# Optimization experiments

Hardware: AMD Instinct MI355X
Metric: run time of the kernel (lower is better)

Reference implementation:

```python
import jax, jax.numpy as jnp
import numpy as np

L, B, E, H, HID = 2048, 4, 512, 8, 2048
HD = E // H


def setup_inputs() -> dict:
    key = jax.random.key(0)
    ks = jax.random.split(key, 6)
    s = 0.02
    x = jax.random.normal(ks[0], (L, B, E), jnp.float32)
    in_proj_w = jax.random.normal(ks[1], (3 * E, E), jnp.float32) * s
    in_proj_b = jnp.zeros((3 * E,), jnp.float32)
    out_w = jax.random.normal(ks[2], (E, E), jnp.float32) * s
    out_b = jnp.zeros((E,), jnp.float32)
    w1 = jax.random.normal(ks[3], (HID, E), jnp.float32) * s  # torch Linear: (out, in)
    b1 = jnp.zeros((HID,), jnp.float32)
    w2 = jax.random.normal(ks[4], (E, HID), jnp.float32) * s
    b2 = jnp.zeros((E,), jnp.float32)
    ln_g = jnp.ones((E,), jnp.float32)
    ln_b = jnp.zeros((E,), jnp.float32)
    return {"x": x, "in_proj_w": in_proj_w, "in_proj_b": in_proj_b,
            "out_w": out_w, "out_b": out_b, "w1": w1, "b1": b1,
            "w2": w2, "b2": b2, "ln_g": ln_g, "ln_b": ln_b}


def _pos_encoding(S, Emb, dtype):
    # even i: sin((t+1) * 10000^(-i/E)); odd i: cos((t+1) * 10000^(-(i+1)/E))
    t = jnp.arange(S, dtype=dtype)[:, None]
    i = jnp.arange(Emb, dtype=dtype)[None, :]
    even = jnp.sin((t + 1.0) * jnp.power(10000.0, -i / Emb))
    odd = jnp.cos((t + 1.0) * jnp.power(10000.0, -(i + 1.0) / Emb))
    return jnp.where(jnp.arange(Emb)[None, :] % 2 == 0, even, odd)  # (S, Emb)


def _layernorm(x, g, b, eps=1e-5):
    mu = jnp.mean(x, axis=-1, keepdims=True)
    var = jnp.mean(jnp.square(x - mu), axis=-1, keepdims=True)
    return (x - mu) * jax.lax.rsqrt(var + eps) * g + b


def _mha(x, in_proj_w, in_proj_b, out_w, out_b):
    # x: (L, B, E); self-attention, torch MultiheadAttention semantics
    qkv = jnp.einsum('lbe,fe->lbf', x, in_proj_w) + in_proj_b
    q, k, v = jnp.split(qkv, 3, axis=-1)
    q = q.reshape(L, B, H, HD)
    k = k.reshape(L, B, H, HD)
    v = v.reshape(L, B, H, HD)
    scores = jnp.einsum('lbhd,mbhd->bhlm', q, k) / np.sqrt(HD).astype(np.float32)
    attn = jax.nn.softmax(scores, axis=-1)
    o = jnp.einsum('bhlm,mbhd->lbhd', attn, v).reshape(L, B, E)
    return jnp.einsum('lbe,fe->lbf', o, out_w) + out_b


def reference(x, in_proj_w, in_proj_b, out_w, out_b, w1, b1, w2, b2, ln_g, ln_b):
    # positional encoding: varies along dim1, broadcasts along dim0 (as in source)
    pe = _pos_encoding(x.shape[1], x.shape[2], x.dtype)  # (B, E)
    x = x + pe[None, :, :]
    # Post-Norm path
    x = _layernorm(_mha(x, in_proj_w, in_proj_b, out_w, out_b) + x, ln_g, ln_b)
    h = jax.nn.gelu(jnp.einsum('lbe,he->lbh', x, w1) + b1, approximate=False)
    ff = jnp.einsum('lbh,eh->lbe', h, w2) + b2
    x = _layernorm(ff + x, ln_g, ln_b)
    return x
```

## Files before the change

### kernel.cpp

```cpp
#include <hip/hip_runtime.h>

typedef unsigned short u16;
typedef unsigned int   u32;
typedef u16  u16x2 __attribute__((ext_vector_type(2)));
typedef u16  u16x4 __attribute__((ext_vector_type(4)));
typedef u16  u16x8 __attribute__((ext_vector_type(8)));
typedef short s8v  __attribute__((ext_vector_type(8)));
typedef short s4v  __attribute__((ext_vector_type(4)));
typedef float f4v  __attribute__((ext_vector_type(4)));
typedef u32  u32x2 __attribute__((ext_vector_type(2)));

#define L_SEQ 2048
#define B_SZ  4
#define E_DIM 512
#define H_CNT 8
#define HD    64
#define HID   2048
#define M_ROWS (L_SEQ * B_SZ)
#define QSCALE 0.18033688011112042f

__device__ __forceinline__ u16 f2b(float f) {
    unsigned u = __builtin_bit_cast(unsigned, f);
    u += 0x7fffu + ((u >> 16) & 1u);
    return (u16)(u >> 16);
}
__device__ __forceinline__ float b2f(u16 u) {
    u32 x = ((u32)u) << 16; return __builtin_bit_cast(float, x);
}
__device__ __forceinline__ u32 pk_trunc(float a, float b) {
    u32 ua = __builtin_bit_cast(u32, a), ub = __builtin_bit_cast(u32, b);
    return (ua >> 16) | (ub & 0xffff0000u);
}
__device__ __forceinline__ void gload_lds16(const u16* g, u16* l) {
    __builtin_amdgcn_global_load_lds((__attribute__((address_space(1))) void*)(u16*)g,
                                     (__attribute__((address_space(3))) void*)l, 16, 0, 0);
}

__global__ __launch_bounds__(256) void pe_tab_k(float* __restrict__ pet) {
    int i = blockIdx.x * 256 + threadIdx.x;
    int e = i & (E_DIM - 1);
    float t = (float)(i >> 9) + 1.0f;
    int ee = (e & 1) ? (e + 1) : e;
    float w = exp2f((-(float)ee / 512.0f) * 13.287712379549449f);
    pet[i] = (e & 1) ? cosf(t * w) : sinf(t * w);
}

__global__ __launch_bounds__(256) void pe_add_k(const float* __restrict__ x,
                                                const float* __restrict__ pet,
                                                u16* __restrict__ xpb) {
    int idx = (blockIdx.x * 256 + threadIdx.x) * 4;
    f4v v = *(const f4v*)(x + idx);
    f4v p = *(const f4v*)(pet + (idx & 2047));
    u16x4 o;
#pragma unroll
    for (int i = 0; i < 4; ++i) o[i] = f2b(v[i] + p[i]);
    *(u16x4*)(xpb + idx) = o;
}

__global__ __launch_bounds__(256) void conv4_k(const float* __restrict__ s1, u16* __restrict__ d1, int n1,
                                               const float* __restrict__ s2, u16* __restrict__ d2, int n2,
                                               const float* __restrict__ s3, u16* __restrict__ d3, int n3,
                                               const float* __restrict__ s4, u16* __restrict__ d4) {
    int o = (blockIdx.x * 256 + threadIdx.x) * 4;
    const float* s; u16* d;
    if (o < n1) { s = s1; d = d1; }
    else { o -= n1;
        if (o < n2) { s = s2; d = d2; }
        else { o -= n2;
            if (o < n3) { s = s3; d = d3; }
            else { o -= n3; s = s4; d = d4; } } }
    f4v v = *(const f4v*)(s + o);
    u16x4 q;
#pragma unroll
    for (int i = 0; i < 4; ++i) q[i] = f2b(v[i]);
    *(u16x4*)(d + o) = q;
}

template <int NP, bool WRITEF, bool WRITEB>
__global__ __launch_bounds__(256)
void ln_c(const u16* __restrict__ p0, const u16* __restrict__ p1,
          const u16* __restrict__ p2, const u16* __restrict__ p3,
          const float* __restrict__ bias, const u16* __restrict__ resid,
          const float* __restrict__ gw, const float* __restrict__ bw,
          float* __restrict__ outF, u16* __restrict__ outB) {
    int wave = threadIdx.x >> 6, lane = threadIdx.x & 63;
    size_t row = (size_t)blockIdx.x * 4 + wave;
    size_t off = row * E_DIM + lane * 8;
    u16x8 rv = *(const u16x8*)(resid + off);
    f4v a, b;
#pragma unroll
    for (int i = 0; i < 4; ++i) { a[i] = b2f(rv[i]); b[i] = b2f(rv[i + 4]); }
    a += *(const f4v*)(bias + lane * 8);
    b += *(const f4v*)(bias + lane * 8 + 4);
    const u16* ps[4] = {p0, p1, p2, p3};
#pragma unroll
    for (int z = 0; z < NP; ++z) {
        u16x8 t = *(const u16x8*)(ps[z] + off);
#pragma unroll
        for (int i = 0; i < 4; ++i) { a[i] += b2f(t[i]); b[i] += b2f(t[i + 4]); }
    }
    float s = (a[0] + a[1]) + (a[2] + a[3]) + (b[0] + b[1]) + (b[2] + b[3]);
#pragma unroll
    for (int o = 1; o < 64; o <<= 1) s += __shfl_xor(s, o, 64);
    float mu = s * (1.0f / E_DIM);
    float q = 0.f;
#pragma unroll
    for (int i = 0; i < 4; ++i) { float d = a[i] - mu; q += d * d; }
#pragma unroll
    for (int i = 0; i < 4; ++i) { float d = b[i] - mu; q += d * d; }
#pragma unroll
    for (int o = 1; o < 64; o <<= 1) q += __shfl_xor(q, o, 64);
    float rstd = rsqrtf(q * (1.0f / E_DIM) + 1e-5f);
    f4v g0 = *(const f4v*)(gw + lane * 8), g1 = *(const f4v*)(gw + lane * 8 + 4);
    f4v w0 = *(const f4v*)(bw + lane * 8), w1 = *(const f4v*)(bw + lane * 8 + 4);
    f4v y0, y1;
#pragma unroll
    for (int i = 0; i < 4; ++i) { y0[i] = (a[i] - mu) * rstd * g0[i] + w0[i];
                                  y1[i] = (b[i] - mu) * rstd * g1[i] + w1[i]; }
    if (WRITEF) {
        *(f4v*)(outF + off)     = y0;
        *(f4v*)(outF + off + 4) = y1;
    }
    if (WRITEB) {
        u16x8 o;
#pragma unroll
        for (int i = 0; i < 4; ++i) { o[i] = f2b(y0[i]); o[i + 4] = f2b(y1[i]); }
        *(u16x8*)(outB + off) = o;
    }
}

__global__ __launch_bounds__(256) void transpose_v_k(const u16* __restrict__ vb,
                                                     u16* __restrict__ vt) {
    __shared__ __align__(16) u16 T[64 * 66];
    int t = threadIdx.x;
    int lt = blockIdx.x, bh = blockIdx.y;
    const u16* src = vb + (size_t)bh * (L_SEQ * HD) + (size_t)lt * 64 * HD;
    int lr = t >> 2, d0 = (t & 3) * 16;
    s8v va = *(const s8v*)(src + lr * HD + d0);
    s8v vb8 = *(const s8v*)(src + lr * HD + d0 + 8);
#pragma unroll
    for (int c = 0; c < 4; ++c) {
        u16x2 p0; p0[0] = (u16)va[c * 2]; p0[1] = (u16)va[c * 2 + 1];
        u16x2 p1; p1[0] = (u16)vb8[c * 2]; p1[1] = (u16)vb8[c * 2 + 1];
        *(u16x2*)(&T[lr * 66 + d0 + c * 2])     = p0;
        *(u16x2*)(&T[lr * 66 + d0 + 8 + c * 2]) = p1;
    }
    __syncthreads();
    int d = t >> 2, l0 = (t & 3) * 16;
    u16 tmp[16];
#pragma unroll
    for (int i = 0; i < 16; ++i) tmp[i] = T[(l0 + i) * 66 + d];
    u16* dst = vt + (size_t)bh * (L_SEQ * HD) + (size_t)d * L_SEQ + lt * 64 + l0;
    u16x8 o0, o1;
#pragma unroll
    for (int i = 0; i < 8; ++i) { o0[i] = tmp[i]; o1[i] = tmp[8 + i]; }
    *(u16x8*)dst       = o0;
    *(u16x8*)(dst + 8) = o1;
}

template <int MODE>
__global__ __launch_bounds__(256, 3)
void gemm_bt(const u16* __restrict__ A, const u16* __restrict__ Bw,
             const float* __restrict__ bias, int M, int N, int K,
             u16* __restrict__ outB,
             u16* __restrict__ oq, u16* __restrict__ okk, u16* __restrict__ ov) {
    __shared__ __align__(16) u16 As[2][128 * 32];
    __shared__ __align__(16) u16 Bs[2][128 * 32];
    const int tid = threadIdx.x;
    const int wave = tid >> 6, lane = tid & 63;
    const int col = lane & 15, quad = lane >> 4;
    const int bm = blockIdx.y * 128, bn = blockIdx.x * 128;
    const int wm = (wave >> 1) * 64, wn = (wave & 1) * 64;
    f4v acc[4][4] = {};
    const int srow = wave * 16 + (lane >> 2);
    const int soff = (lane & 3) * 8;
    const u16* Ag = A + (size_t)(bm + srow) * K + soff;
    const u16* Bg = Bw + (size_t)(bn + srow) * K + soff;
    const int wo = wave * 512;
    for (int kc = 0; kc < K; kc += 64) {
        __syncthreads();
#pragma unroll
        for (int hs = 0; hs < 2; ++hs) {
            gload_lds16(Ag + kc + hs * 32,                  &As[hs][wo]);
            gload_lds16(Ag + (size_t)64 * K + kc + hs * 32, &As[hs][wo + 2048]);
            gload_lds16(Bg + kc + hs * 32,                  &Bs[hs][wo]);
            gload_lds16(Bg + (size_t)64 * K + kc + hs * 32, &Bs[hs][wo + 2048]);
        }
        __syncthreads();
#pragma unroll
        for (int hs = 0; hs < 2; ++hs) {
            s8v af[4], bf[4];
#pragma unroll
            for (int i = 0; i < 4; ++i) af[i] = *(const s8v*)(&As[hs][(wm + i * 16 + col) * 32 + quad * 8]);
#pragma unroll
            for (int j = 0; j < 4; ++j) bf[j] = *(const s8v*)(&Bs[hs][(wn + j * 16 + col) * 32 + quad * 8]);
#pragma unroll
            for (int i = 0; i < 4; ++i)
#pragma unroll
                for (int j = 0; j < 4; ++j)
                    acc[i][j] = __builtin_amdgcn_mfma_f32_16x16x32_bf16(af[i], bf[j], acc[i][j], 0, 0, 0);
        }
    }
#pragma unroll
    for (int j = 0; j < 4; ++j) {
        int gn = bn + wn + j * 16 + col;
        float bv = bias[gn];
#pragma unroll
        for (int i = 0; i < 4; ++i) {
            int gm0 = bm + wm + i * 16 + quad * 4;
#pragma unroll
            for (int r = 0; r < 4; ++r) {
                float v = acc[i][j][r] + bv;
                int m = gm0 + r;
                if (MODE == 2) {
                    float gel = 0.5f * v * (1.0f + erff(v * 0.70710678118654752f));
                    outB[(size_t)m * N + gn] = f2b(gel);
                } else {
                    int l = m >> 2, bb = m & 3;
                    int which = gn >> 9, hh = (gn >> 6) & 7, d = gn & 63;
                    u16* dst = (which == 0) ? oq : ((which == 1) ? okk : ov);
                    if (which == 0) v *= QSCALE;
                    dst[((size_t)(bb * H_CNT + hh) * L_SEQ + l) * HD + d] = f2b(v);
                }
            }
        }
    }
}

__global__ __launch_bounds__(256, 3)
void gemm_ks(const u16* __restrict__ A, const u16* __restrict__ Bw,
             int N, int K, int Kper,
             u16* __restrict__ q0, u16* __restrict__ q1,
             u16* __restrict__ q2, u16* __restrict__ q3) {
    __shared__ __align__(16) u16 As[2][128 * 32];
    __shared__ __align__(16) u16 Bs[2][128 * 32];
    const int tid = threadIdx.x;
    const int wave = tid >> 6, lane = tid & 63;
    const int col = lane & 15, quad = lane >> 4;
    const int bm = blockIdx.y * 128, bn = blockIdx.x * 128;
    const int kz = blockIdx.z;
    u16* pz = (kz == 0) ? q0 : (kz == 1) ? q1 : (kz == 2) ? q2 : q3;
    const int wm = (wave >> 1) * 64, wn = (wave & 1) * 64;
    f4v acc[4][4] = {};
    const int srow = wave * 16 + (lane >> 2);
    const int soff = (lane & 3) * 8;
    const u16* Ag = A + (size_t)(bm + srow) * K + kz * Kper + soff;
    const u16* Bg = Bw + (size_t)(bn + srow) * K + kz * Kper + soff;
    const int wo = wave * 512;
    for (int kc = 0; kc < Kper; kc += 64) {
        __syncthreads();
#pragma unroll
        for (int hs = 0; hs < 2; ++hs) {
            gload_lds16(Ag + kc + hs * 32,                  &As[hs][wo]);
            gload_lds16(Ag + (size_t)64 * K + kc + hs * 32, &As[hs][wo + 2048]);
            gload_lds16(Bg + kc + hs * 32,                  &Bs[hs][wo]);
            gload_lds16(Bg + (size_t)64 * K + kc + hs * 32, &Bs[hs][wo + 2048]);
        }
        __syncthreads();
#pragma unroll
        for (int hs = 0; hs < 2; ++hs) {
            s8v af[4], bf[4];
#pragma unroll
            for (int i = 0; i < 4; ++i) af[i] = *(const s8v*)(&As[hs][(wm + i * 16 + col) * 32 + quad * 8]);
#pragma unroll
            for (int j = 0; j < 4; ++j) bf[j] = *(const s8v*)(&Bs[hs][(wn + j * 16 + col) * 32 + quad * 8]);
#pragma unroll
            for (int i = 0; i < 4; ++i)
#pragma unroll
                for (int j = 0; j < 4; ++j)
                    acc[i][j] = __builtin_amdgcn_mfma_f32_16x16x32_bf16(af[i], bf[j], acc[i][j], 0, 0, 0);
        }
    }
#pragma unroll
    for (int j = 0; j < 4; ++j) {
        int gn = bn + wn + j * 16 + col;
#pragma unroll
        for (int i = 0; i < 4; ++i) {
            int m0 = bm + wm + i * 16 + quad * 4;
#pragma unroll
            for (int r = 0; r < 4; ++r)
                pz[(size_t)(m0 + r) * N + gn] = f2b(acc[i][j][r]);
        }
    }
}

__global__ __launch_bounds__(256, 4)
void attn_k(const u16* __restrict__ qg, const u16* __restrict__ kg,
            const u16* __restrict__ vtg,
            u16* __restrict__ po0, u16* __restrict__ po1,
            u16* __restrict__ po2, u16* __restrict__ po3, float* __restrict__ lbuf) {
    __shared__ __align__(16) u16 Ks[2][2][64 * 32];
    __shared__ __align__(16) u16 Vs[2][2][64 * 32];
    const int tid = threadIdx.x;
    const int wave = tid >> 6, lane = tid & 63;
    const int col = lane & 15, quad = lane >> 4;
    const int qc = blockIdx.x, kz = blockIdx.y, bh = blockIdx.z;
    const size_t base = (size_t)bh * (L_SEQ * HD);
    s8v qf[2][2];
#pragma unroll
    for (int t = 0; t < 2; ++t) {
        const int qrow = qc * 128 + wave * 32 + t * 16 + col;
#pragma unroll
        for (int hh = 0; hh < 2; ++hh)
            qf[t][hh] = *(const s8v*)(qg + base + (size_t)qrow * HD + hh * 32 + quad * 8);
    }
    f4v oa[2][4] = {};
    f4v la[2] = {};
    const s4v vones = {0x3F80, 0x3F80, 0x3F80, 0x3F80};
    const int h = wave & 1, r0 = (wave >> 1) * 16;
    const int srow = lane >> 2, c = lane & 3;
    const int cp = c ^ ((srow >> 1) & 3);
    const u16* Kg = kg + base + (size_t)(r0 + srow) * HD + h * 32 + cp * 8;
    const u16* Vg = vtg + base + (size_t)(r0 + srow) * L_SEQ + h * 32 + cp * 8;
    const int kt0 = kz * 8;
    {
        const int kv0 = kt0 * 64;
        gload_lds16(Kg + (size_t)kv0 * HD,        &Ks[0][h][r0 * 32]);
        gload_lds16(Kg + (size_t)(kv0 + 32) * HD, &Ks[0][h][(r0 + 32) * 32]);
        gload_lds16(Vg + kv0,                     &Vs[0][h][r0 * 32]);
        gload_lds16(Vg + kv0 + (size_t)32 * L_SEQ,&Vs[0][h][(r0 + 32) * 32]);
    }
    const int perm = (col >> 1) & 3;
    for (int it = 0; it < 8; ++it) {
        const int cur = it & 1, nxt = cur ^ 1;
        __syncthreads();
        if (it + 1 < 8) {
            const int kv0 = (kt0 + it + 1) * 64;
            gload_lds16(Kg + (size_t)kv0 * HD,        &Ks[nxt][h][r0 * 32]);
            gload_lds16(Kg + (size_t)(kv0 + 32) * HD, &Ks[nxt][h][(r0 + 32) * 32]);
            gload_lds16(Vg + kv0,                     &Vs[nxt][h][r0 * 32]);
            gload_lds16(Vg + kv0 + (size_t)32 * L_SEQ,&Vs[nxt][h][(r0 + 32) * 32]);
        }
        f4v st[2][4];
#pragma unroll
        for (int j = 0; j < 4; ++j) {
            s8v k0 = *(const s8v*)(&Ks[cur][0][(j * 16 + col) * 32 + ((quad ^ perm) * 8)]);
            s8v k1 = *(const s8v*)(&Ks[cur][1][(j * 16 + col) * 32 + ((quad ^ perm) * 8)]);
#pragma unroll
            for (int t = 0; t < 2; ++t) {
                f4v z = {};
                z = __builtin_amdgcn_mfma_f32_16x16x32_bf16(k0, qf[t][0], z, 0, 0, 0);
                z = __builtin_amdgcn_mfma_f32_16x16x32_bf16(k1, qf[t][1], z, 0, 0, 0);
                st[t][j] = z;
            }
        }
        s4v pt[2][4];
#pragma unroll
        for (int t = 0; t < 2; ++t)
#pragma unroll
            for (int j = 0; j < 4; ++j) {
                f4v p;
#pragma unroll
                for (int r = 0; r < 4; ++r) p[r] = exp2f(st[t][j][r]);
                u32x2 pk;
                pk[0] = pk_trunc(p[0], p[1]);
                pk[1] = pk_trunc(p[2], p[3]);
                pt[t][j] = __builtin_bit_cast(s4v, pk);
            }
#pragma unroll
        for (int cc = 0; cc < 4; ++cc) {
            const int hh = cc >> 1;
            const int ch8 = (cc & 1) * 2 + (quad >> 1);
#pragma unroll
            for (int dj = 0; dj < 4; ++dj) {
                s4v vf = *(const s4v*)(&Vs[cur][hh][(dj * 16 + col) * 32 + ((ch8 ^ perm) * 8) + (quad & 1) * 4]);
#pragma unroll
                for (int t = 0; t < 2; ++t)
                    oa[t][dj] = __builtin_amdgcn_mfma_f32_16x16x16bf16_1k(pt[t][cc], vf, oa[t][dj], 0, 0, 0);
            }
#pragma unroll
            for (int t = 0; t < 2; ++t)
                la[t] = __builtin_amdgcn_mfma_f32_16x16x16bf16_1k(pt[t][cc], vones, la[t], 0, 0, 0);
        }
    }
    if (col == 0) {
#pragma unroll
        for (int t = 0; t < 2; ++t)
#pragma unroll
            for (int r = 0; r < 4; ++r)
                lbuf[kz * 65536 + bh * 2048 + (qc * 128 + wave * 32 + t * 16 + quad * 4 + r)] = la[t][r];
    }
    u16* pg = (kz == 0) ? po0 : (kz == 1) ? po1 : (kz == 2) ? po2 : po3;
    const int b = bh >> 3, hd = bh & 7;
#pragma unroll
    for (int t = 0; t < 2; ++t)
#pragma unroll
        for (int r = 0; r < 4; ++r) {
            int lrow = qc * 128 + wave * 32 + t * 16 + quad * 4 + r;
            size_t mrow = (size_t)(lrow * 4 + b) * E_DIM + hd * HD;
#pragma unroll
            for (int dj = 0; dj < 4; ++dj)
                pg[mrow + dj * 16 + col] = f2b(oa[t][dj][r]);
        }
}

__global__ __launch_bounds__(256)
void combine_k(const u16* __restrict__ p0, const u16* __restrict__ p1,
               const u16* __restrict__ p2, const u16* __restrict__ p3,
               const float* __restrict__ lbuf, u16* __restrict__ out) {
    int idx8 = blockIdx.x * 256 + threadIdx.x;
    int m = idx8 >> 6;
    int e0 = (idx8 & 63) * 8;
    int b = m & 3, lrow = m >> 2, h = e0 >> 6;
    int li = (b * 8 + h) * 2048 + lrow;
    float inv = 1.0f / (lbuf[li] + lbuf[65536 + li] + lbuf[131072 + li] + lbuf[196608 + li]);
    size_t off = (size_t)m * E_DIM + e0;
    u16x8 a0 = *(const u16x8*)(p0 + off);
    u16x8 a1 = *(const u16x8*)(p1 + off);
    u16x8 a2 = *(const u16x8*)(p2 + off);
    u16x8 a3 = *(const u16x8*)(p3 + off);
    u16x8 o;
#pragma unroll
    for (int i = 0; i < 8; ++i)
        o[i] = f2b(((b2f(a0[i]) + b2f(a1[i])) + (b2f(a2[i]) + b2f(a3[i]))) * inv);
    *(u16x8*)(out + off) = o;
}

extern "C" void kernel_launch(void* const* d_in, const int* in_sizes, int n_in,
                              void* d_out, int out_size, void* d_ws, size_t ws_size,
                              hipStream_t stream) {
    const float* x     = (const float*)d_in[0];
    const float* w_qkv = (const float*)d_in[1];
    const float* b_qkv = (const float*)d_in[2];
    const float* w_out = (const float*)d_in[3];
    const float* b_out = (const float*)d_in[4];
    const float* w1    = (const float*)d_in[5];
    const float* b1    = (const float*)d_in[6];
    const float* w2    = (const float*)d_in[7];
    const float* b2    = (const float*)d_in[8];
    const float* ln_g  = (const float*)d_in[9];
    const float* ln_b  = (const float*)d_in[10];

    char* ws = (char*)d_ws;
    u16*   WQKV = (u16*)(ws + 0);
    u16*   WOUT = (u16*)(ws + 1572864);
    u16*   W1B  = (u16*)(ws + 2097152);
    u16*   W2B  = (u16*)(ws + 4194304);
    u16*   XPB  = (u16*)(ws + 6291456);
    u16*   QB   = (u16*)(ws + 14680064);
    u16*   KB   = (u16*)(ws + 23068672);
    u16*   VB   = (u16*)(ws + 31457280);
    u16*   VT   = (u16*)(ws + 39845888);
    u16*   AP0  = (u16*)(ws + 48234496);
    u16*   AP1  = (u16*)(ws + 56623104);
    u16*   AP2  = (u16*)(ws + 65011712);
    u16*   AP3  = (u16*)(ws + 73400320);
    float* LB   = (float*)(ws + 81788928);
    float* PET  = (float*)(ws + 82837504);
    u16*   OB   = VB;
    u16*   OP0  = (u16*)(ws + 48234496);
    u16*   OP1  = (u16*)(ws + 56623104);
    u16*   X3B  = QB;
    u16*   HB   = (u16*)(ws + 48234496);
    u16*   FP0  = XPB;
    u16*   FP1  = KB;

    pe_tab_k<<<8, 256, 0, stream>>>(PET);
    pe_add_k<<<4096, 256, 0, stream>>>(x, PET, XPB);
    conv4_k<<<3072, 256, 0, stream>>>(w_qkv, WQKV, 3 * E_DIM * E_DIM,
                                      w_out, WOUT, E_DIM * E_DIM,
                                      w1, W1B, HID * E_DIM,
                                      w2, W2B);
    gemm_bt<0><<<dim3(12, 64), 256, 0, stream>>>(XPB, WQKV, b_qkv, M_ROWS, 3 * E_DIM, E_DIM,
                                                 nullptr, QB, KB, VB);
    transpose_v_k<<<dim3(32, 32), 256, 0, stream>>>(VB, VT);
    attn_k<<<dim3(16, 4, 32), 256, 0, stream>>>(QB, KB, VT, AP0, AP1, AP2, AP3, LB);
    combine_k<<<2048, 256, 0, stream>>>(AP0, AP1, AP2, AP3, LB, OB);
    gemm_ks<<<dim3(4, 64, 2), 256, 0, stream>>>(OB, WOUT, E_DIM, E_DIM, 256,
                                                OP0, OP1, nullptr, nullptr);
    ln_c<2, false, true><<<2048, 256, 0, stream>>>(OP0, OP1, nullptr, nullptr,
                                                   b_out, XPB, ln_g, ln_b, nullptr, X3B);
    gemm_bt<2><<<dim3(16, 64), 256, 0, stream>>>(X3B, W1B, b1, M_ROWS, HID, E_DIM,
                                                 HB, nullptr, nullptr, nullptr);
    gemm_ks<<<dim3(4, 64, 2), 256, 0, stream>>>(HB, W2B, E_DIM, HID, 1024,
                                                FP0, FP1, nullptr, nullptr);
    ln_c<2, true, false><<<2048, 256, 0, stream>>>(FP0, FP1, nullptr, nullptr,
                                                   b2, X3B, ln_g, ln_b, (float*)d_out, nullptr);
}
```

Before: 273.5 us.

## Double-buffer LDS tiles in GEMM kernels to overlap loads with MFMA

Both tiled GEMM kernels (gemm_bt and gemm_ks) now keep two LDS stages. The first K-chunk is prefetched before the loop, and the next chunk's global-to-LDS copies are issued before the MFMAs on the current chunk. This removes one barrier per iteration and aims to hide global load latency behind matrix math. In exchange, LDS per block doubles to 64KB and launch bounds drop from 3 to 2 blocks per CU, which lowers occupancy. The overlap also depends on the async LDS loads not being forced to complete before the compute starts.

```diff
diff --git a/kernel.cpp b/kernel.cpp
--- a/kernel.cpp
+++ b/kernel.cpp
@@ -159,13 +159,13 @@
 }
 
 template <int MODE>
-__global__ __launch_bounds__(256, 3)
+__global__ __launch_bounds__(256, 2)
 void gemm_bt(const u16* __restrict__ A, const u16* __restrict__ Bw,
              const float* __restrict__ bias, int M, int N, int K,
              u16* __restrict__ outB,
              u16* __restrict__ oq, u16* __restrict__ okk, u16* __restrict__ ov) {
-    __shared__ __align__(16) u16 As[2][128 * 32];
-    __shared__ __align__(16) u16 Bs[2][128 * 32];
+    __shared__ __align__(16) u16 As[2][2][128 * 32];
+    __shared__ __align__(16) u16 Bs[2][2][128 * 32];
     const int tid = threadIdx.x;
     const int wave = tid >> 6, lane = tid & 63;
     const int col = lane & 15, quad = lane >> 4;
@@ -177,23 +177,34 @@
     const u16* Ag = A + (size_t)(bm + srow) * K + soff;
     const u16* Bg = Bw + (size_t)(bn + srow) * K + soff;
     const int wo = wave * 512;
-    for (int kc = 0; kc < K; kc += 64) {
+#pragma unroll
+    for (int hs = 0; hs < 2; ++hs) {
+        gload_lds16(Ag + hs * 32,                  &As[0][hs][wo]);
+        gload_lds16(Ag + (size_t)64 * K + hs * 32, &As[0][hs][wo + 2048]);
+        gload_lds16(Bg + hs * 32,                  &Bs[0][hs][wo]);
+        gload_lds16(Bg + (size_t)64 * K + hs * 32, &Bs[0][hs][wo + 2048]);
+    }
+    const int nit = K >> 6;
+    for (int t = 0; t < nit; ++t) {
+        const int cur = t & 1, nxt = cur ^ 1;
         __syncthreads();
-#pragma unroll
-        for (int hs = 0; hs < 2; ++hs) {
-            gload_lds16(Ag + kc + hs * 32,                  &As[hs][wo]);
-            gload_lds16(Ag + (size_t)64 * K + kc + hs * 32, &As[hs][wo + 2048]);
-            gload_lds16(Bg + kc + hs * 32,                  &Bs[hs][wo]);
-            gload_lds16(Bg + (size_t)64 * K + kc + hs * 32, &Bs[hs][wo + 2048]);
-        }
-        __syncthreads();
+        if (t + 1 < nit) {
+            const int kc = (t + 1) * 64;
+#pragma unroll
+            for (int hs = 0; hs < 2; ++hs) {
+                gload_lds16(Ag + kc + hs * 32,                  &As[nxt][hs][wo]);
+                gload_lds16(Ag + (size_t)64 * K + kc + hs * 32, &As[nxt][hs][wo + 2048]);
+                gload_lds16(Bg + kc + hs * 32,                  &Bs[nxt][hs][wo]);
+                gload_lds16(Bg + (size_t)64 * K + kc + hs * 32, &Bs[nxt][hs][wo + 2048]);
+            }
+        }
 #pragma unroll
         for (int hs = 0; hs < 2; ++hs) {
             s8v af[4], bf[4];
 #pragma unroll
-            for (int i = 0; i < 4; ++i) af[i] = *(const s8v*)(&As[hs][(wm + i * 16 + col) * 32 + quad * 8]);
-#pragma unroll
-            for (int j = 0; j < 4; ++j) bf[j] = *(const s8v*)(&Bs[hs][(wn + j * 16 + col) * 32 + quad * 8]);
+            for (int i = 0; i < 4; ++i) af[i] = *(const s8v*)(&As[cur][hs][(wm + i * 16 + col) * 32 + quad * 8]);
+#pragma unroll
+            for (int j = 0; j < 4; ++j) bf[j] = *(const s8v*)(&Bs[cur][hs][(wn + j * 16 + col) * 32 + quad * 8]);
 #pragma unroll
             for (int i = 0; i < 4; ++i)
 #pragma unroll
@@ -227,13 +238,13 @@
     }
 }
 
-__global__ __launch_bounds__(256, 3)
+__global__ __launch_bounds__(256, 2)
 void gemm_ks(const u16* __restrict__ A, const u16* __restrict__ Bw,
              int N, int K, int Kper,
              u16* __restrict__ q0, u16* __restrict__ q1,
              u16* __restrict__ q2, u16* __restrict__ q3) {
-    __shared__ __align__(16) u16 As[2][128 * 32];
-    __shared__ __align__(16) u16 Bs[2][128 * 32];
+    __shared__ __align__(16) u16 As[2][2][128 * 32];
+    __shared__ __align__(16) u16 Bs[2][2][128 * 32];
     const int tid = threadIdx.x;
     const int wave = tid >> 6, lane = tid & 63;
     const int col = lane & 15, quad = lane >> 4;
@@ -247,23 +258,34 @@
     const u16* Ag = A + (size_t)(bm + srow) * K + kz * Kper + soff;
     const u16* Bg = Bw + (size_t)(bn + srow) * K + kz * Kper + soff;
     const int wo = wave * 512;
-    for (int kc = 0; kc < Kper; kc += 64) {
+#pragma unroll
+    for (int hs = 0; hs < 2; ++hs) {
+        gload_lds16(Ag + hs * 32,                  &As[0][hs][wo]);
+        gload_lds16(Ag + (size_t)64 * K + hs * 32, &As[0][hs][wo + 2048]);
+        gload_lds16(Bg + hs * 32,                  &Bs[0][hs][wo]);
+        gload_lds16(Bg + (size_t)64 * K + hs * 32, &Bs[0][hs][wo + 2048]);
+    }
+    const int nit = Kper >> 6;
+    for (int t = 0; t < nit; ++t) {
+        const int cur = t & 1, nxt = cur ^ 1;
         __syncthreads();
-#pragma unroll
-        for (int hs = 0; hs < 2; ++hs) {
-            gload_lds16(Ag + kc + hs * 32,                  &As[hs][wo]);
-            gload_lds16(Ag + (size_t)64 * K + kc + hs * 32, &As[hs][wo + 2048]);
-            gload_lds16(Bg + kc + hs * 32,                  &Bs[hs][wo]);
-            gload_lds16(Bg + (size_t)64 * K + kc + hs * 32, &Bs[hs][wo + 2048]);
-        }
-        __syncthreads();
+        if (t + 1 < nit) {
+            const int kc = (t + 1) * 64;
+#pragma unroll
+            for (int hs = 0; hs < 2; ++hs) {
+                gload_lds16(Ag + kc + hs * 32,                  &As[nxt][hs][wo]);
+                gload_lds16(Ag + (size_t)64 * K + kc + hs * 32, &As[nxt][hs][wo + 2048]);
+                gload_lds16(Bg + kc + hs * 32,                  &Bs[nxt][hs][wo]);
+                gload_lds16(Bg + (size_t)64 * K + kc + hs * 32, &Bs[nxt][hs][wo + 2048]);
+            }
+        }
 #pragma unroll
         for (int hs = 0; hs < 2; ++hs) {
             s8v af[4], bf[4];
 #pragma unroll
-            for (int i = 0; i < 4; ++i) af[i] = *(const s8v*)(&As[hs][(wm + i * 16 + col) * 32 + quad * 8]);
-#pragma unroll
-            for (int j = 0; j < 4; ++j) bf[j] = *(const s8v*)(&Bs[hs][(wn + j * 16 + col) * 32 + quad * 8]);
+            for (int i = 0; i < 4; ++i) af[i] = *(const s8v*)(&As[cur][hs][(wm + i * 16 + col) * 32 + quad * 8]);
+#pragma unroll
+            for (int j = 0; j < 4; ++j) bf[j] = *(const s8v*)(&Bs[cur][hs][(wn + j * 16 + col) * 32 + quad * 8]);
 #pragma unroll
             for (int i = 0; i < 4; ++i)
 #pragma unroll
```

After: 277.2 us. Within noise of the previous version (+1.4%).
